# Kernel optimization log

Hardware: AMD Instinct MI355X
Metric: run time of the kernel (lower is better)

## Reference

```python
import jax, jax.numpy as jnp
import numpy as np
from jax import lax

# Mamba hyperparams implied by Mamba(d_model=8, d_state=16, d_conv=4, expand=2)
D_MODEL, D_STATE, D_CONV, EXPAND = 8, 16, 4, 2
D_INNER = EXPAND * D_MODEL          # 16
DT_RANK = -(-D_MODEL // 16)          # ceil(8/16) = 1
BATCH, SEQ_LEN, NUM_CLASSES = 1024, 250, 12


def silu(v):
    return v * jax.nn.sigmoid(v)


def setup_inputs() -> dict:
    key = jax.random.key(0)
    ks = jax.random.split(key, 12)
    s = 0.05
    return {
        "x": jax.random.normal(ks[0], (BATCH, D_MODEL, SEQ_LEN), jnp.float32),
        "in_proj_w": jax.random.normal(ks[1], (2 * D_INNER, D_MODEL), jnp.float32) * s,
        "conv_w": jax.random.normal(ks[2], (D_INNER, D_CONV), jnp.float32) * s,
        "conv_b": jax.random.normal(ks[3], (D_INNER,), jnp.float32) * s,
        "x_proj_w": jax.random.normal(ks[4], (DT_RANK + 2 * D_STATE, D_INNER), jnp.float32) * s,
        "dt_proj_w": jax.random.normal(ks[5], (D_INNER, DT_RANK), jnp.float32) * s,
        "dt_proj_b": jax.random.normal(ks[6], (D_INNER,), jnp.float32) * s,
        "A_log": jnp.log(jnp.tile(jnp.arange(1, D_STATE + 1, dtype=jnp.float32), (D_INNER, 1))),
        "D": jnp.ones((D_INNER,), jnp.float32),
        "out_proj_w": jax.random.normal(ks[7], (D_MODEL, D_INNER), jnp.float32) * s,
        "fc_w": jax.random.normal(ks[8], (NUM_CLASSES, D_MODEL * SEQ_LEN), jnp.float32) * s,
        "fc_b": jax.random.normal(ks[9], (NUM_CLASSES,), jnp.float32) * s,
    }


def reference(x, in_proj_w, conv_w, conv_b, x_proj_w, dt_proj_w, dt_proj_b,
              A_log, D, out_proj_w, fc_w, fc_b):
    B = x.shape[0]
    xt = jnp.transpose(x, (0, 2, 1))                       # (B, L, d_model)
    xz = xt @ in_proj_w.T                                  # (B, L, 2*d_inner)
    x_in, z = xz[..., :D_INNER], xz[..., D_INNER:]

    # causal depthwise conv1d along time, kernel d_conv, padding d_conv-1, crop to L
    xp = jnp.pad(x_in, ((0, 0), (D_CONV - 1, 0), (0, 0)))  # (B, L+3, d_inner)
    acc = conv_b
    for k in range(D_CONV):  # small fixed kernel loop
        acc = acc + conv_w[:, k] * xp[:, k:k + SEQ_LEN, :]
    u = silu(acc)                                          # (B, L, d_inner)

    x_dbl = u @ x_proj_w.T                                 # (B, L, dt_rank+2*d_state)
    dt = x_dbl[..., :DT_RANK]
    Bm = x_dbl[..., DT_RANK:DT_RANK + D_STATE]             # (B, L, d_state)
    Cm = x_dbl[..., DT_RANK + D_STATE:]                    # (B, L, d_state)
    delta = jax.nn.softplus(dt @ dt_proj_w.T + dt_proj_b)  # (B, L, d_inner)

    A = -jnp.exp(A_log)                                    # (d_inner, d_state)
    dA = jnp.exp(delta[..., None] * A)                     # (B, L, d_inner, d_state)
    dBu = delta[..., None] * Bm[:, :, None, :] * u[..., None]

    def step(h, inp):
        dA_t, dBu_t, C_t = inp
        h = dA_t * h + dBu_t                               # (B, d_inner, d_state)
        y_t = jnp.einsum('bds,bs->bd', h, C_t)
        return h, y_t

    h0 = jnp.zeros((B, D_INNER, D_STATE), x.dtype)
    _, ys = lax.scan(step, h0, (jnp.moveaxis(dA, 1, 0),
                                jnp.moveaxis(dBu, 1, 0),
                                jnp.moveaxis(Cm, 1, 0)))
    y = jnp.moveaxis(ys, 0, 1) + u * D                     # (B, L, d_inner)
    y = y * silu(z)
    out = y @ out_proj_w.T                                 # (B, L, d_model)

    flat = out.reshape(B, D_MODEL * SEQ_LEN)
    return flat @ fc_w.T + fc_b                            # (B, num_classes)
```

## Files before the change

### kernel.cpp

```cpp
#include <hip/hip_runtime.h>
#include <hip/hip_fp16.h>
#include <math.h>

#define SEQ 250
#define ST  252
#define NCLS 12

typedef __attribute__((ext_vector_type(4))) _Float16 half4v;
typedef __attribute__((ext_vector_type(4))) float    float4v;

template<int CTRL>
__device__ __forceinline__ float dpp_add(float v) {
    int t = __builtin_amdgcn_update_dpp(0, __float_as_int(v), CTRL, 0xF, 0xF, true);
    return v + __int_as_float(t);
}

__device__ __forceinline__ __half2 f_as_h2(float f) {
    union { float f; __half2 h; } u; u.f = f; return u.h;
}
__device__ __forceinline__ float h2_as_f(__half2 h) {
    union { __half2 h; float f; } u; u.h = h; return u.f;
}

__global__ __launch_bounds__(512)
void mamba_cls_kernel(
    const float* __restrict__ x,
    const float* __restrict__ in_proj_w,
    const float* __restrict__ conv_w,
    const float* __restrict__ conv_b,
    const float* __restrict__ x_proj_w,
    const float* __restrict__ dt_proj_w,
    const float* __restrict__ dt_proj_b,
    const float* __restrict__ A_log,
    const float* __restrict__ Dp,
    const float* __restrict__ out_proj_w,
    const float* __restrict__ fc_w,
    const float* __restrict__ fc_b,
    float* __restrict__ out)
{
    __shared__ __align__(16) __half2 s_bc [2][16 * ST];
    __shared__ __align__(16) __half2 s_dlu[2][16 * ST];
    __shared__ __align__(16) __half  s_sz [2][16 * ST];

    const int tid  = threadIdx.x;
    const int p    = tid >> 8;
    const int tid8 = tid & 255;
    const int b0   = blockIdx.x * 2;

    {
        float* s_xf = (float*)s_dlu[0];
        const float* __restrict__ xb = x + (size_t)b0 * (8 * SEQ);
        for (int i = tid; i < 2 * 8 * SEQ; i += 512) s_xf[i] = xb[i];
    }
    __syncthreads();

    {
        float* s_f  = (float*)s_bc[p];
        const float* s_xf = (const float*)s_dlu[0] + p * (8 * SEQ);
        const int d  = tid8 & 15;
        const int t0 = tid8 >> 4;
        float w1[8], w2[8];
        #pragma unroll
        for (int m = 0; m < 8; ++m) {
            w1[m] = in_proj_w[d * 8 + m];
            w2[m] = in_proj_w[(16 + d) * 8 + m];
        }
        #pragma unroll
        for (int i = 0; i < 16; ++i) {
            int t = t0 + i * 16;
            if (t < SEQ) {
                float acc = 0.f, z = 0.f;
                #pragma unroll
                for (int m = 0; m < 8; ++m) {
                    float xv = s_xf[m * SEQ + t];
                    acc = fmaf(w1[m], xv, acc);
                    z   = fmaf(w2[m], xv, z);
                }
                s_f[d * ST + t] = acc;
                s_sz[p][d * ST + t] = __float2half(z / (1.f + __expf(-z)));
            }
        }
    }
    __syncthreads();

    {
        const float* s_f = (const float*)s_bc[p];
        const int d  = tid8 & 15;
        const int t0 = tid8 >> 4;
        float cw[4];
        #pragma unroll
        for (int k = 0; k < 4; ++k) cw[k] = conv_w[d * 4 + k];
        const float cb = conv_b[d];
        #pragma unroll
        for (int i = 0; i < 16; ++i) {
            int t = t0 + i * 16;
            if (t < SEQ) {
                float acc = cb;
                #pragma unroll
                for (int k = 0; k < 4; ++k) {
                    int tt = t + k - 3;
                    if (tt >= 0) acc = fmaf(cw[k], s_f[d * ST + tt], acc);
                }
                float sg = 1.f / (1.f + __expf(-acc));
                s_dlu[p][d * ST + t].y = __float2half(acc * sg);
            }
        }
    }
    __syncthreads();

    {
        const int wave = tid8 >> 6;
        const int l    = tid8 & 63;
        const int rowc = l & 15;
        const int kg   = l >> 4;

        half4v wB, wC, wD;
        #pragma unroll
        for (int i = 0; i < 4; ++i) {
            wB[i] = (_Float16)x_proj_w[(1  + rowc) * 16 + 4 * kg + i];
            wC[i] = (_Float16)x_proj_w[(17 + rowc) * 16 + 4 * kg + i];
            wD[i] = (_Float16)x_proj_w[4 * kg + i];
        }
        const float dtw_c = dt_proj_w[rowc];
        const float dtb_c = dt_proj_b[rowc];
        const float4v zero4 = {0.f, 0.f, 0.f, 0.f};
        const unsigned int* __restrict__ dlu_w = (const unsigned int*)s_dlu[p];

        for (int tile = wave; tile < 16; tile += 4) {
            const int t0 = tile * 16;
            unsigned int w0 = dlu_w[(4 * kg + 0) * ST + t0 + rowc];
            unsigned int w1 = dlu_w[(4 * kg + 1) * ST + t0 + rowc];
            unsigned int w2 = dlu_w[(4 * kg + 2) * ST + t0 + rowc];
            unsigned int w3 = dlu_w[(4 * kg + 3) * ST + t0 + rowc];
            union { unsigned int u[2]; half4v h; } A;
            A.u[0] = (w0 >> 16) | (w1 & 0xFFFF0000u);
            A.u[1] = (w2 >> 16) | (w3 & 0xFFFF0000u);

            float4v dB = __builtin_amdgcn_mfma_f32_16x16x16f16(A.h, wB, zero4, 0, 0, 0);
            float4v dC = __builtin_amdgcn_mfma_f32_16x16x16f16(A.h, wC, zero4, 0, 0, 0);
            float4v dT = __builtin_amdgcn_mfma_f32_16x16x16f16(A.h, wD, zero4, 0, 0, 0);

            const int tb = t0 + kg * 4;
            if (tb <= 248) {
                __half2 h0 = __floats2half2_rn(dB[0], dC[0]);
                __half2 h1 = __floats2half2_rn(dB[1], dC[1]);
                __half2 h2 = __floats2half2_rn(dB[2], dC[2]);
                __half2 h3 = __floats2half2_rn(dB[3], dC[3]);
                float4 wv;
                wv.x = h2_as_f(h0); wv.y = h2_as_f(h1);
                wv.z = h2_as_f(h2); wv.w = h2_as_f(h3);
                *reinterpret_cast<float4*>(s_bc[p] + rowc * ST + tb) = wv;
            }
            #pragma unroll
            for (int r = 0; r < 4; ++r) {
                int t = tb + r;
                if (t < SEQ) {
                    float v  = fmaf(dT[r], dtw_c, dtb_c);
                    float dl = (v > 20.f) ? v : __logf(1.f + __expf(v));
                    s_dlu[p][rowc * ST + t].x = __float2half(dl);
                }
            }
        }
    }
    __syncthreads();

    if (tid < 256) {
        const int sp   = tid >> 7;
        const int i7   = tid & 127;
        const int d    = i7 >> 3;
        const int s2   = i7 & 7;
        const float A2a = -__expf(A_log[d * 16 + s2])     * 1.4426950408889634f;
        const float A2b = -__expf(A_log[d * 16 + s2 + 8]) * 1.4426950408889634f;
        const float Dd  = Dp[d];
        const __half2* __restrict__ dlu_p = s_dlu[sp] + d * ST;
        const __half2* __restrict__ bca_p = s_bc [sp] + s2 * ST;
        const __half2* __restrict__ bcb_p = s_bc [sp] + (s2 + 8) * ST;
        const __half*  __restrict__ sz_p  = (const __half*)s_sz[sp] + d * ST;
        float* __restrict__ y_p = (float*)s_dlu[sp] + d * ST;
        float ha = 0.f, hb = 0.f;
        for (int t = 0; t < 248; t += 4) {
            float4 duv4 = *reinterpret_cast<const float4*>(dlu_p + t);
            float4 bca4 = *reinterpret_cast<const float4*>(bca_p + t);
            float4 bcb4 = *reinterpret_cast<const float4*>(bcb_p + t);
            float2 sz2  = *reinterpret_cast<const float2*>(sz_p + t);
            float fdu[4] = {duv4.x, duv4.y, duv4.z, duv4.w};
            float fba[4] = {bca4.x, bca4.y, bca4.z, bca4.w};
            float fbb[4] = {bcb4.x, bcb4.y, bcb4.z, bcb4.w};
            float2 szl = __half22float2(f_as_h2(sz2.x));
            float2 szh = __half22float2(f_as_h2(sz2.y));
            float fsz[4] = {szl.x, szl.y, szh.x, szh.y};
            #pragma unroll
            for (int tt = 0; tt < 4; ++tt) {
                float2 du  = __half22float2(f_as_h2(fdu[tt]));
                float2 bca = __half22float2(f_as_h2(fba[tt]));
                float2 bcb = __half22float2(f_as_h2(fbb[tt]));
                float dlu = du.x * du.y;
                ha = fmaf(exp2f(du.x * A2a), ha, dlu * bca.x);
                hb = fmaf(exp2f(du.x * A2b), hb, dlu * bcb.x);
                float r = fmaf(hb, bcb.y, ha * bca.y);
                r = dpp_add<0xB1>(r);
                r = dpp_add<0x4E>(r);
                r = dpp_add<0x141>(r);
                if (s2 == 0) y_p[t + tt] = fmaf(du.y, Dd, r) * fsz[tt];
            }
        }
        {
            float2 duv2 = *reinterpret_cast<const float2*>(dlu_p + 248);
            float2 bca2 = *reinterpret_cast<const float2*>(bca_p + 248);
            float2 bcb2 = *reinterpret_cast<const float2*>(bcb_p + 248);
            float2 szf  = __half22float2(*reinterpret_cast<const __half2*>(sz_p + 248));
            float fdu[2] = {duv2.x, duv2.y};
            float fba[2] = {bca2.x, bca2.y};
            float fbb[2] = {bcb2.x, bcb2.y};
            float fsz[2] = {szf.x, szf.y};
            #pragma unroll
            for (int tt = 0; tt < 2; ++tt) {
                float2 du  = __half22float2(f_as_h2(fdu[tt]));
                float2 bca = __half22float2(f_as_h2(fba[tt]));
                float2 bcb = __half22float2(f_as_h2(fbb[tt]));
                float dlu = du.x * du.y;
                ha = fmaf(exp2f(du.x * A2a), ha, dlu * bca.x);
                hb = fmaf(exp2f(du.x * A2b), hb, dlu * bcb.x);
                float r = fmaf(hb, bcb.y, ha * bca.y);
                r = dpp_add<0xB1>(r);
                r = dpp_add<0x4E>(r);
                r = dpp_add<0x141>(r);
                if (s2 == 0) y_p[248 + tt] = fmaf(du.y, Dd, r) * fsz[tt];
            }
        }
    }
    __syncthreads();

    {
        float* s_f  = (float*)s_bc[p];
        const float* s_yf = (const float*)s_dlu[p];
        const int j = tid8 & 7;
        float w[16];
        #pragma unroll
        for (int d2 = 0; d2 < 16; ++d2) w[d2] = out_proj_w[j * 16 + d2];
        for (int t0 = (tid8 >> 3) * 4; t0 < SEQ; t0 += 128) {
            float a0 = 0.f, a1 = 0.f, a2 = 0.f, a3 = 0.f;
            #pragma unroll
            for (int d2 = 0; d2 < 16; ++d2) {
                float4 y4 = *reinterpret_cast<const float4*>(s_yf + d2 * ST + t0);
                a0 = fmaf(w[d2], y4.x, a0);
                a1 = fmaf(w[d2], y4.y, a1);
                a2 = fmaf(w[d2], y4.z, a2);
                a3 = fmaf(w[d2], y4.w, a3);
            }
            s_f[(t0 + 0) * 8 + j] = a0;
            s_f[(t0 + 1) * 8 + j] = a1;
            if (t0 + 2 < SEQ) s_f[(t0 + 2) * 8 + j] = a2;
            if (t0 + 3 < SEQ) s_f[(t0 + 3) * 8 + j] = a3;
        }
    }
    __syncthreads();

    {
        float* s_yf = (float*)s_dlu[p];
        float p_[NCLS];
        #pragma unroll
        for (int c = 0; c < NCLS; ++c) p_[c] = 0.f;
        const float4* fw4 = (const float4*)fc_w;
        const float4* sf4 = (const float4*)s_bc[p];
        for (int q = tid8; q < 500; q += 256) {
            float4 f = sf4[q];
            #pragma unroll
            for (int c = 0; c < NCLS; ++c) {
                float4 wv = fw4[c * 500 + q];
                p_[c] += f.x * wv.x + f.y * wv.y + f.z * wv.z + f.w * wv.w;
            }
        }
        #pragma unroll
        for (int c = 0; c < NCLS; ++c) {
            float v = p_[c];
            v = dpp_add<0xB1>(v);
            v = dpp_add<0x4E>(v);
            v = dpp_add<0x141>(v);
            v = dpp_add<0x140>(v);
            v += __shfl_xor(v, 16);
            v += __shfl_xor(v, 32);
            p_[c] = v;
        }
        const int wave = tid8 >> 6;
        const int lane = tid8 & 63;
        __syncthreads();
        if (lane == 0) {
            #pragma unroll
            for (int c = 0; c < NCLS; ++c) s_yf[wave * NCLS + c] = p_[c];
        }
        __syncthreads();
        if (tid8 < NCLS) {
            float v = s_yf[tid8] + s_yf[NCLS + tid8] + s_yf[2 * NCLS + tid8] +
                      s_yf[3 * NCLS + tid8] + fc_b[tid8];
            out[(size_t)(b0 + p) * NCLS + tid8] = v;
        }
    }
}

extern "C" void kernel_launch(void* const* d_in, const int* in_sizes, int n_in,
                              void* d_out, int out_size, void* d_ws, size_t ws_size,
                              hipStream_t stream) {
    const float* x          = (const float*)d_in[0];
    const float* in_proj_w  = (const float*)d_in[1];
    const float* conv_w     = (const float*)d_in[2];
    const float* conv_b     = (const float*)d_in[3];
    const float* x_proj_w   = (const float*)d_in[4];
    const float* dt_proj_w  = (const float*)d_in[5];
    const float* dt_proj_b  = (const float*)d_in[6];
    const float* A_log      = (const float*)d_in[7];
    const float* Dp         = (const float*)d_in[8];
    const float* out_proj_w = (const float*)d_in[9];
    const float* fc_w       = (const float*)d_in[10];
    const float* fc_b       = (const float*)d_in[11];
    float* out = (float*)d_out;

    const int batch = in_sizes[0] / (8 * SEQ);
    mamba_cls_kernel<<<batch / 2, 512, 0, stream>>>(
        x, in_proj_w, conv_w, conv_b, x_proj_w, dt_proj_w, dt_proj_b,
        A_log, Dp, out_proj_w, fc_w, fc_b, out);
}
```

Before: 54.84 us.

## Use MFMA for in_proj, vectorize x load and conv stage

```diff
diff --git a/kernel.cpp b/kernel.cpp
--- a/kernel.cpp
+++ b/kernel.cpp
@@ -48,62 +48,86 @@
     const int b0   = blockIdx.x * 2;
 
     {
-        float* s_xf = (float*)s_dlu[0];
-        const float* __restrict__ xb = x + (size_t)b0 * (8 * SEQ);
-        for (int i = tid; i < 2 * 8 * SEQ; i += 512) s_xf[i] = xb[i];
-    }
-    __syncthreads();
-
-    {
-        float* s_f  = (float*)s_bc[p];
+        float4* s_xf4 = (float4*)s_dlu[0];
+        const float4* __restrict__ xb4 =
+            (const float4*)(x + (size_t)b0 * (8 * SEQ));
+        for (int i = tid; i < 1000; i += 512) s_xf4[i] = xb4[i];
+    }
+    __syncthreads();
+
+    {
+        const int l    = tid8 & 63;
+        const int rowc = l & 15;
+        const int kg   = l >> 4;
+        const int wave = tid8 >> 6;
+        half4v wX, wZ;
+        #pragma unroll
+        for (int i = 0; i < 4; ++i) {
+            int k = 4 * kg + i;
+            wX[i] = (k < 8) ? (_Float16)in_proj_w[rowc * 8 + k] : (_Float16)0.f;
+            wZ[i] = (k < 8) ? (_Float16)in_proj_w[(16 + rowc) * 8 + k] : (_Float16)0.f;
+        }
         const float* s_xf = (const float*)s_dlu[0] + p * (8 * SEQ);
+        float* s_f = (float*)s_bc[p];
+        __half* szp = (__half*)s_sz[p];
+        const float4v zero4 = {0.f, 0.f, 0.f, 0.f};
+        const int ksafe = 4 * (kg & 1);
+        for (int tile = wave; tile < 16; tile += 4) {
+            const int t0 = tile * 16;
+            half4v A;
+            #pragma unroll
+            for (int i = 0; i < 4; ++i)
+                A[i] = (_Float16)s_xf[(ksafe + i) * SEQ + t0 + rowc];
+            float4v dX = __builtin_amdgcn_mfma_f32_16x16x16f16(A, wX, zero4, 0, 0, 0);
+            float4v dZ = __builtin_amdgcn_mfma_f32_16x16x16f16(A, wZ, zero4, 0, 0, 0);
+            const int tb = t0 + kg * 4;
+            if (tb <= 248) {
+                float4 xw;
+                xw.x = dX[0]; xw.y = dX[1]; xw.z = dX[2]; xw.w = dX[3];
+                *reinterpret_cast<float4*>(s_f + rowc * ST + tb) = xw;
+                float sz0 = dZ[0] / (1.f + __expf(-dZ[0]));
+                float sz1 = dZ[1] / (1.f + __expf(-dZ[1]));
+                float sz2 = dZ[2] / (1.f + __expf(-dZ[2]));
+                float sz3 = dZ[3] / (1.f + __expf(-dZ[3]));
+                float2 zw;
+                zw.x = h2_as_f(__floats2half2_rn(sz0, sz1));
+                zw.y = h2_as_f(__floats2half2_rn(sz2, sz3));
+                *reinterpret_cast<float2*>(szp + rowc * ST + tb) = zw;
+            }
+        }
+    }
+    __syncthreads();
+
+    {
         const int d  = tid8 & 15;
-        const int t0 = tid8 >> 4;
-        float w1[8], w2[8];
-        #pragma unroll
-        for (int m = 0; m < 8; ++m) {
-            w1[m] = in_proj_w[d * 8 + m];
-            w2[m] = in_proj_w[(16 + d) * 8 + m];
-        }
-        #pragma unroll
-        for (int i = 0; i < 16; ++i) {
-            int t = t0 + i * 16;
-            if (t < SEQ) {
-                float acc = 0.f, z = 0.f;
-                #pragma unroll
-                for (int m = 0; m < 8; ++m) {
-                    float xv = s_xf[m * SEQ + t];
-                    acc = fmaf(w1[m], xv, acc);
-                    z   = fmaf(w2[m], xv, z);
-                }
-                s_f[d * ST + t] = acc;
-                s_sz[p][d * ST + t] = __float2half(z / (1.f + __expf(-z)));
-            }
-        }
-    }
-    __syncthreads();
-
-    {
-        const float* s_f = (const float*)s_bc[p];
-        const int d  = tid8 & 15;
-        const int t0 = tid8 >> 4;
+        const int c0 = (tid8 >> 4) * 4;
         float cw[4];
         #pragma unroll
         for (int k = 0; k < 4; ++k) cw[k] = conv_w[d * 4 + k];
         const float cb = conv_b[d];
-        #pragma unroll
-        for (int i = 0; i < 16; ++i) {
-            int t = t0 + i * 16;
-            if (t < SEQ) {
+        const float* s_f = (const float*)s_bc[p] + d * ST;
+        __half2* dluw = s_dlu[p] + d * ST;
+        const __half hz = __float2half(0.f);
+        for (int t0 = c0; t0 < SEQ; t0 += 64) {
+            float w[8];
+            if (t0 == 0) {
+                w[0] = 0.f; w[1] = 0.f; w[2] = 0.f; w[3] = 0.f;
+            } else {
+                float4 a = *reinterpret_cast<const float4*>(s_f + t0 - 4);
+                w[0] = a.x; w[1] = a.y; w[2] = a.z; w[3] = a.w;
+            }
+            float4 bv = *reinterpret_cast<const float4*>(s_f + t0);
+            w[4] = bv.x; w[5] = bv.y; w[6] = bv.z; w[7] = bv.w;
+            float4 uw;
+            #pragma unroll
+            for (int j = 0; j < 4; ++j) {
                 float acc = cb;
                 #pragma unroll
-                for (int k = 0; k < 4; ++k) {
-                    int tt = t + k - 3;
-                    if (tt >= 0) acc = fmaf(cw[k], s_f[d * ST + tt], acc);
-                }
+                for (int k = 0; k < 4; ++k) acc = fmaf(cw[k], w[j + k + 1], acc);
                 float sg = 1.f / (1.f + __expf(-acc));
-                s_dlu[p][d * ST + t].y = __float2half(acc * sg);
-            }
+                ((float*)&uw)[j] = h2_as_f(__halves2half2(hz, __float2half(acc * sg)));
+            }
+            *reinterpret_cast<float4*>(dluw + t0) = uw;
         }
     }
     __syncthreads();
```

New measurement: 56.00 us. +2.1%, slower.

## Remap scan to four states per lane with double-buffered LDS loads

Applied to the files above, without the earlier changes.

```diff
diff --git a/kernel.cpp b/kernel.cpp
--- a/kernel.cpp
+++ b/kernel.cpp
@@ -48,9 +48,10 @@
     const int b0   = blockIdx.x * 2;
 
     {
-        float* s_xf = (float*)s_dlu[0];
-        const float* __restrict__ xb = x + (size_t)b0 * (8 * SEQ);
-        for (int i = tid; i < 2 * 8 * SEQ; i += 512) s_xf[i] = xb[i];
+        float4* s_xf4 = (float4*)s_dlu[0];
+        const float4* __restrict__ xb4 =
+            (const float4*)(x + (size_t)b0 * (8 * SEQ));
+        for (int i = tid; i < 1000; i += 512) s_xf4[i] = xb4[i];
     }
     __syncthreads();
 
@@ -164,68 +165,122 @@
     }
     __syncthreads();
 
-    if (tid < 256) {
-        const int sp   = tid >> 7;
-        const int i7   = tid & 127;
-        const int d    = i7 >> 3;
-        const int s2   = i7 & 7;
-        const float A2a = -__expf(A_log[d * 16 + s2])     * 1.4426950408889634f;
-        const float A2b = -__expf(A_log[d * 16 + s2 + 8]) * 1.4426950408889634f;
+    if (tid < 128) {
+        const int sp = tid >> 6;
+        const int l  = tid & 63;
+        const int d  = l >> 2;
+        const int s2 = l & 3;
+        const float LOG2E = 1.4426950408889634f;
+        const float A20 = -__expf(A_log[d * 16 + s2])      * LOG2E;
+        const float A21 = -__expf(A_log[d * 16 + s2 + 4])  * LOG2E;
+        const float A22 = -__expf(A_log[d * 16 + s2 + 8])  * LOG2E;
+        const float A23 = -__expf(A_log[d * 16 + s2 + 12]) * LOG2E;
         const float Dd  = Dp[d];
         const __half2* __restrict__ dlu_p = s_dlu[sp] + d * ST;
-        const __half2* __restrict__ bca_p = s_bc [sp] + s2 * ST;
-        const __half2* __restrict__ bcb_p = s_bc [sp] + (s2 + 8) * ST;
+        const __half2* __restrict__ bc0_p = s_bc [sp] + s2 * ST;
+        const __half2* __restrict__ bc1_p = s_bc [sp] + (s2 + 4) * ST;
+        const __half2* __restrict__ bc2_p = s_bc [sp] + (s2 + 8) * ST;
+        const __half2* __restrict__ bc3_p = s_bc [sp] + (s2 + 12) * ST;
         const __half*  __restrict__ sz_p  = (const __half*)s_sz[sp] + d * ST;
         float* __restrict__ y_p = (float*)s_dlu[sp] + d * ST;
-        float ha = 0.f, hb = 0.f;
-        for (int t = 0; t < 248; t += 4) {
-            float4 duv4 = *reinterpret_cast<const float4*>(dlu_p + t);
-            float4 bca4 = *reinterpret_cast<const float4*>(bca_p + t);
-            float4 bcb4 = *reinterpret_cast<const float4*>(bcb_p + t);
-            float2 sz2  = *reinterpret_cast<const float2*>(sz_p + t);
-            float fdu[4] = {duv4.x, duv4.y, duv4.z, duv4.w};
-            float fba[4] = {bca4.x, bca4.y, bca4.z, bca4.w};
-            float fbb[4] = {bcb4.x, bcb4.y, bcb4.z, bcb4.w};
-            float2 szl = __half22float2(f_as_h2(sz2.x));
-            float2 szh = __half22float2(f_as_h2(sz2.y));
-            float fsz[4] = {szl.x, szl.y, szh.x, szh.y};
-            #pragma unroll
-            for (int tt = 0; tt < 4; ++tt) {
-                float2 du  = __half22float2(f_as_h2(fdu[tt]));
-                float2 bca = __half22float2(f_as_h2(fba[tt]));
-                float2 bcb = __half22float2(f_as_h2(fbb[tt]));
+        float h0 = 0.f, h1 = 0.f, h2 = 0.f, h3 = 0.f;
+
+        float4 A_du, A_b0, A_b1, A_b2, A_b3;
+        float4 B_du, B_b0, B_b1, B_b2, B_b3;
+        float2 A_sz, B_sz;
+
+#define SCAN_LOAD(buf, tt) do { \
+        buf##_du = *reinterpret_cast<const float4*>(dlu_p + (tt)); \
+        buf##_b0 = *reinterpret_cast<const float4*>(bc0_p + (tt)); \
+        buf##_b1 = *reinterpret_cast<const float4*>(bc1_p + (tt)); \
+        buf##_b2 = *reinterpret_cast<const float4*>(bc2_p + (tt)); \
+        buf##_b3 = *reinterpret_cast<const float4*>(bc3_p + (tt)); \
+        buf##_sz = *reinterpret_cast<const float2*>(sz_p + (tt)); } while (0)
+
+#define SCAN_COMPUTE(buf, tt) do { \
+        float fdu[4] = {buf##_du.x, buf##_du.y, buf##_du.z, buf##_du.w}; \
+        float fb0[4] = {buf##_b0.x, buf##_b0.y, buf##_b0.z, buf##_b0.w}; \
+        float fb1[4] = {buf##_b1.x, buf##_b1.y, buf##_b1.z, buf##_b1.w}; \
+        float fb2[4] = {buf##_b2.x, buf##_b2.y, buf##_b2.z, buf##_b2.w}; \
+        float fb3[4] = {buf##_b3.x, buf##_b3.y, buf##_b3.z, buf##_b3.w}; \
+        float2 szl = __half22float2(f_as_h2(buf##_sz.x)); \
+        float2 szh = __half22float2(f_as_h2(buf##_sz.y)); \
+        float fsz[4] = {szl.x, szl.y, szh.x, szh.y}; \
+        float yv[4]; \
+        _Pragma("unroll") \
+        for (int q = 0; q < 4; ++q) { \
+            float2 du = __half22float2(f_as_h2(fdu[q])); \
+            float2 b0 = __half22float2(f_as_h2(fb0[q])); \
+            float2 b1 = __half22float2(f_as_h2(fb1[q])); \
+            float2 b2 = __half22float2(f_as_h2(fb2[q])); \
+            float2 b3 = __half22float2(f_as_h2(fb3[q])); \
+            float dlu = du.x * du.y; \
+            h0 = fmaf(exp2f(du.x * A20), h0, dlu * b0.x); \
+            h1 = fmaf(exp2f(du.x * A21), h1, dlu * b1.x); \
+            h2 = fmaf(exp2f(du.x * A22), h2, dlu * b2.x); \
+            h3 = fmaf(exp2f(du.x * A23), h3, dlu * b3.x); \
+            float r = h0 * b0.y; \
+            r = fmaf(h1, b1.y, r); \
+            r = fmaf(h2, b2.y, r); \
+            r = fmaf(h3, b3.y, r); \
+            r = dpp_add<0xB1>(r); \
+            r = dpp_add<0x4E>(r); \
+            yv[q] = fmaf(du.y, Dd, r) * fsz[q]; \
+        } \
+        if (s2 == 0) { \
+            float4 y4; y4.x = yv[0]; y4.y = yv[1]; y4.z = yv[2]; y4.w = yv[3]; \
+            *reinterpret_cast<float4*>(y_p + (tt)) = y4; \
+        } } while (0)
+
+        SCAN_LOAD(A, 0);
+        for (int t = 0; t < 240; t += 8) {
+            SCAN_LOAD(B, t + 4);
+            SCAN_COMPUTE(A, t);
+            SCAN_LOAD(A, t + 8);
+            SCAN_COMPUTE(B, t + 4);
+        }
+        SCAN_LOAD(B, 244);
+        SCAN_COMPUTE(A, 240);
+        SCAN_COMPUTE(B, 244);
+#undef SCAN_LOAD
+#undef SCAN_COMPUTE
+        {
+            float2 duv2 = *reinterpret_cast<const float2*>(dlu_p + 248);
+            float2 b0v  = *reinterpret_cast<const float2*>(bc0_p + 248);
+            float2 b1v  = *reinterpret_cast<const float2*>(bc1_p + 248);
+            float2 b2v  = *reinterpret_cast<const float2*>(bc2_p + 248);
+            float2 b3v  = *reinterpret_cast<const float2*>(bc3_p + 248);
+            float2 szf  = __half22float2(*reinterpret_cast<const __half2*>(sz_p + 248));
+            float fdu[2] = {duv2.x, duv2.y};
+            float fb0[2] = {b0v.x, b0v.y};
+            float fb1[2] = {b1v.x, b1v.y};
+            float fb2[2] = {b2v.x, b2v.y};
+            float fb3[2] = {b3v.x, b3v.y};
+            float fsz[2] = {szf.x, szf.y};
+            float yv[2];
+            #pragma unroll
+            for (int q = 0; q < 2; ++q) {
+                float2 du = __half22float2(f_as_h2(fdu[q]));
+                float2 b0 = __half22float2(f_as_h2(fb0[q]));
+                float2 b1 = __half22float2(f_as_h2(fb1[q]));
+                float2 b2 = __half22float2(f_as_h2(fb2[q]));
+                float2 b3 = __half22float2(f_as_h2(fb3[q]));
                 float dlu = du.x * du.y;
-                ha = fmaf(exp2f(du.x * A2a), ha, dlu * bca.x);
-                hb = fmaf(exp2f(du.x * A2b), hb, dlu * bcb.x);
-                float r = fmaf(hb, bcb.y, ha * bca.y);
+                h0 = fmaf(exp2f(du.x * A20), h0, dlu * b0.x);
+                h1 = fmaf(exp2f(du.x * A21), h1, dlu * b1.x);
+                h2 = fmaf(exp2f(du.x * A22), h2, dlu * b2.x);
+                h3 = fmaf(exp2f(du.x * A23), h3, dlu * b3.x);
+                float r = h0 * b0.y;
+                r = fmaf(h1, b1.y, r);
+                r = fmaf(h2, b2.y, r);
+                r = fmaf(h3, b3.y, r);
                 r = dpp_add<0xB1>(r);
                 r = dpp_add<0x4E>(r);
-                r = dpp_add<0x141>(r);
-                if (s2 == 0) y_p[t + tt] = fmaf(du.y, Dd, r) * fsz[tt];
-            }
-        }
-        {
-            float2 duv2 = *reinterpret_cast<const float2*>(dlu_p + 248);
-            float2 bca2 = *reinterpret_cast<const float2*>(bca_p + 248);
-            float2 bcb2 = *reinterpret_cast<const float2*>(bcb_p + 248);
-            float2 szf  = __half22float2(*reinterpret_cast<const __half2*>(sz_p + 248));
-            float fdu[2] = {duv2.x, duv2.y};
-            float fba[2] = {bca2.x, bca2.y};
-            float fbb[2] = {bcb2.x, bcb2.y};
-            float fsz[2] = {szf.x, szf.y};
-            #pragma unroll
-            for (int tt = 0; tt < 2; ++tt) {
-                float2 du  = __half22float2(f_as_h2(fdu[tt]));
-                float2 bca = __half22float2(f_as_h2(fba[tt]));
-                float2 bcb = __half22float2(f_as_h2(fbb[tt]));
-                float dlu = du.x * du.y;
-                ha = fmaf(exp2f(du.x * A2a), ha, dlu * bca.x);
-                hb = fmaf(exp2f(du.x * A2b), hb, dlu * bcb.x);
-                float r = fmaf(hb, bcb.y, ha * bca.y);
-                r = dpp_add<0xB1>(r);
-                r = dpp_add<0x4E>(r);
-                r = dpp_add<0x141>(r);
-                if (s2 == 0) y_p[248 + tt] = fmaf(du.y, Dd, r) * fsz[tt];
+                yv[q] = fmaf(du.y, Dd, r) * fsz[q];
+            }
+            if (s2 == 0) {
+                float2 y2; y2.x = yv[0]; y2.y = yv[1];
+                *reinterpret_cast<float2*>(y_p + 248) = y2;
             }
         }
     }
```

Measured after the change: 71.19 us. +29.8%, slower.
